# Kernel optimization log

Hardware: AMD Instinct MI355X
Metric: run time of the kernel (lower is better)

## Reference

```python
import jax, jax.numpy as jnp
import numpy as np

B, N, LATENT, HIDDEN = 65536, 32, 32, 64

def setup_inputs() -> dict:
    key = jax.random.key(0)
    ks = jax.random.split(key, 16)
    def xavier(k, shape):
        fan_in, fan_out = shape[1], shape[0]
        lim = float(np.sqrt(6.0 / (fan_in + fan_out)))
        return jax.random.uniform(k, shape, jnp.float32, -lim, lim)
    inp = {
        'x_sensors': jax.random.normal(ks[0], (B, N), jnp.float32),
        'state_x': jax.random.uniform(ks[1], (B, 1), jnp.float32),
        # GAT: W Linear(1, LATENT, bias=False), a Linear(2*LATENT, 1, bias=False), xavier init
        'W_gat': xavier(ks[2], (LATENT, 1)),
        'a_gat': xavier(ks[3], (1, 2 * LATENT)),
        # pooling: Linear(LATENT, LATENT//2) -> Tanh -> Linear(LATENT//2, 1) -> Softmax(dim=1)
        'p1_w': xavier(ks[4], (LATENT // 2, LATENT)),
        'p1_b': jnp.zeros((LATENT // 2,), jnp.float32),
        'p2_w': xavier(ks[5], (1, LATENT // 2)),
        'p2_b': jnp.zeros((1,), jnp.float32),
        # MNN: MonotonicLinear raw weights uniform(-0.5, 0.5), zero bias
        'm1_w': jax.random.uniform(ks[6], (HIDDEN, 1), jnp.float32, -0.5, 0.5),
        'm1_b': jnp.zeros((HIDDEN,), jnp.float32),
        'm2_w': jax.random.uniform(ks[7], (HIDDEN, HIDDEN), jnp.float32, -0.5, 0.5),
        'm2_b': jnp.zeros((HIDDEN,), jnp.float32),
        'm3_w': jax.random.uniform(ks[8], (LATENT, HIDDEN), jnp.float32, -0.5, 0.5),
        'm3_b': jnp.zeros((LATENT,), jnp.float32),
    }
    return inp

def reference(x_sensors, state_x, W_gat, a_gat, p1_w, p1_b, p2_w, p2_b,
              m1_w, m1_b, m2_w, m2_b, m3_w, m3_b):
    # --- GAT encoder ---
    # h = x_sensors[..., None] (B,N,1); Wh = h @ W_gat.T -> (B,N,D)
    Wh = jnp.einsum('bn,d->bnd', x_sensors, W_gat[:, 0])
    # e_ij = leakyrelu(a^T [Wh_i || Wh_j]) decomposed: a = [a1; a2]
    a1, a2 = a_gat[0, :LATENT], a_gat[0, LATENT:]
    s_i = jnp.einsum('bnd,d->bn', Wh, a1)  # contribution of Wh_i
    s_j = jnp.einsum('bnd,d->bn', Wh, a2)  # contribution of Wh_j
    e = jax.nn.leaky_relu(s_i[:, :, None] + s_j[:, None, :], 0.2)  # (B,N,N)
    alpha = jax.nn.softmax(e, axis=2)  # dropout is identity in eval
    h_prime = jnp.einsum('bij,bjd->bid', alpha, Wh)  # (B,N,D)
    # pooling: softmax over sensor dim (dim=1)
    t = jnp.tanh(h_prime @ p1_w.T + p1_b)
    beta = jax.nn.softmax(t @ p2_w.T + p2_b, axis=1)  # (B,N,1)
    z_enc = jnp.sum(h_prime * beta, axis=1)  # (B,D)
    # --- MNN decoder (exp-positive weights) ---
    h1 = jnp.tanh(state_x @ jnp.exp(m1_w).T + m1_b)
    h2 = jnp.tanh(h1 @ jnp.exp(m2_w).T + m2_b)
    z_dec = h2 @ jnp.exp(m3_w).T + m3_b  # (B,D)
    return (z_enc, z_dec)
```

## Files before the change

### kernel.cpp

```cpp
#include <hip/hip_runtime.h>
#include <hip/hip_bf16.h>

#define LOG2E     1.4426950408889634f
#define TWO_LOG2E 2.8853900817779268f

typedef __attribute__((ext_vector_type(8))) _Float16 f16x8;
typedef __attribute__((ext_vector_type(4))) float    f32x4;
typedef __attribute__((ext_vector_type(2))) float    f32x2;

__device__ __forceinline__ float rcp_(float x){ return __builtin_amdgcn_rcpf(x); }
__device__ __forceinline__ float ex2_(float x){ return __builtin_amdgcn_exp2f(x); }

template<int K>
__device__ __forceinline__ float quadbc(float v){
  constexpr int ctrl = K * 0x55;
  return __int_as_float(__builtin_amdgcn_mov_dpp(__float_as_int(v), ctrl, 0xf, 0xf, true));
}

union FragH { f16x8 v; uint32_t w[4]; uint4 u4; };

__device__ __forceinline__ uint32_t pkh(float a, float b){
  union { _Float16 h; uint16_t u; } ca, cb;
  ca.h = (_Float16)a; cb.h = (_Float16)b;
  return (uint32_t)ca.u | ((uint32_t)cb.u << 16);
}
__device__ __forceinline__ void exph8(const float* __restrict__ src, FragH& out){
  float4 a = *(const float4*)src;
  float4 b = *(const float4*)(src + 4);
  out.w[0] = pkh(__expf(a.x), __expf(a.y));
  out.w[1] = pkh(__expf(a.z), __expf(a.w));
  out.w[2] = pkh(__expf(b.x), __expf(b.y));
  out.w[3] = pkh(__expf(b.z), __expf(b.w));
}

#define WS_FG1   0
#define WS_FG2   2048
#define WS_TBL   3072
#define WS_E1S   3584
#define WS_M1B   3648
#define WS_SCAL  3712

#define TBL_N     512
#define TBL_SCALE 25.6f
#define TBL_LO    -10.0f
#define TBL_CMAX  9.9f

__global__ __launch_bounds__(256) void IDSSM_pre(
    const float* __restrict__ Wg,  const float* __restrict__ ag,
    const float* __restrict__ p1w, const float* __restrict__ p1b,
    const float* __restrict__ p2w, const float* __restrict__ p2b,
    const float* __restrict__ m1w, const float* __restrict__ m1b,
    const float* __restrict__ m2w, const float* __restrict__ m3w,
    float* __restrict__ ws)
{
  const int blk = blockIdx.x;
  const int tid = threadIdx.x;
  const int l  = tid & 63;
  const int bl = l & 15, gt = l >> 4;
  if (blk < 2){
    const int s  = (blk*256 + tid) >> 6;
    const int mt = s >> 1, kt = s & 1;
    FragH h;
    exph8(m2w + (bl + 16*mt)*64 + 8*gt + 32*kt, h);
    *(uint4*)(ws + WS_FG1 + (size_t)(s*64 + l)*4) = h.u4;
  } else if (blk == 2){
    const int s2  = tid >> 6;
    const int mt2 = s2 >> 1, kt2 = s2 & 1;
    FragH h;
    exph8(m3w + (bl + 16*mt2)*64 + 8*gt + 32*kt2, h);
    *(uint4*)(ws + WS_FG2 + (size_t)(s2*64 + l)*4) = h.u4;
  } else if (blk == 3){
    __shared__ float qs[16], pb_[16], pw[16], u0s[1];
    if (tid < 16){
      float acc = 0.f;
      #pragma unroll
      for (int d = 0; d < 32; ++d) acc += p1w[tid*32 + d] * Wg[d];
      qs[tid]  = acc * TWO_LOG2E;
      pb_[tid] = p1b[tid] * TWO_LOG2E;
      pw[tid]  = -2.f * p2w[tid];
    }
    if (tid == 16){
      float sp = 0.f;
      #pragma unroll
      for (int k = 0; k < 16; ++k) sp += p2w[k];
      u0s[0] = sp + p2b[0];
    }
    __syncthreads();
    #pragma unroll
    for (int rep = 0; rep < 2; ++rep){
      const int n = tid + rep*256;
      const float c = TBL_LO + (float)n * (1.0f/TBL_SCALE);
      float u = u0s[0];
      #pragma unroll
      for (int k = 0; k < 16; ++k){
        float E = ex2_(fmaf(c, qs[k], pb_[k]));
        u = fmaf(pw[k], rcp_(E + 1.f), u);
      }
      ws[WS_TBL + n] = u * LOG2E;
    }
  } else {
    if (tid < 64){
      ws[WS_E1S + tid] = __expf(m1w[tid]) * TWO_LOG2E;
      ws[WS_M1B + tid] = m1b[tid] * TWO_LOG2E;
    } else if (tid == 64){
      float A1 = 0.f, A2 = 0.f;
      #pragma unroll
      for (int d = 0; d < 32; ++d){ A1 += Wg[d]*ag[d]; A2 += Wg[d]*ag[32+d]; }
      ws[WS_SCAL + 0] = A1 * LOG2E;
      ws[WS_SCAL + 1] = A2 * LOG2E;
    }
  }
}

#define EATT_J(SX, SF, SQ, JQ, JR) { \
    const float Fj_ = quadbc<JQ>(SF[JR]); \
    const float Fq_ = quadbc<JQ>(SQ[JR]); \
    const float xj_ = quadbc<JQ>(SX[JR]); \
    const f32x2 Fj2_ = {Fj_,Fj_}, Fq2_ = {Fq_,Fq_}, xj2_ = {xj_,xj_}; \
    f32x2 pe_; \
    pe_ = __builtin_elementwise_max(Ei2[0]*Fj2_, Eq2[0]*Fq2_); s2[0] = s2[0] + pe_; sx2[0] = sx2[0] + pe_*xj2_; \
    pe_ = __builtin_elementwise_max(Ei2[1]*Fj2_, Eq2[1]*Fq2_); s2[1] = s2[1] + pe_; sx2[1] = sx2[1] + pe_*xj2_; \
  }
#define EATT_Q(SX, SF, SQ, JQ) \
    EATT_J(SX,SF,SQ,JQ,0) EATT_J(SX,SF,SQ,JQ,1) EATT_J(SX,SF,SQ,JQ,2) EATT_J(SX,SF,SQ,JQ,3)
#define EATT_ALL(SX, SF, SQ) \
    EATT_Q(SX,SF,SQ,0) EATT_Q(SX,SF,SQ,1) EATT_Q(SX,SF,SQ,2) EATT_Q(SX,SF,SQ,3)

__global__ __launch_bounds__(256, 6) void IDSSM_main(
    const float* __restrict__ xs,  const float* __restrict__ stx,
    const float* __restrict__ Wg,  const float* __restrict__ m2b,
    const float* __restrict__ m3b, const float* __restrict__ ws,
    float* __restrict__ out, int B)
{
  __shared__ float tbl[TBL_N];
  const int tid = threadIdx.x;
  const int lb  = tid >> 3;
  const int r   = tid & 7;
  const int b0  = blockIdx.x * 32;
  const int b   = b0 + lb;
  const bool valid = (b < B);
  const int rsrc = valid ? b : (B - 1);

  const float2 tco = *(const float2*)(ws + WS_TBL + tid*2);
  tbl[tid*2]     = tco.x;
  tbl[tid*2 + 1] = tco.y;

  const float A1p = ws[WS_SCAL + 0];
  const float A2p = ws[WS_SCAL + 1];

  const float4 xv = *(const float4*)(xs + (size_t)rsrc*32 + r*4);
  float xi[4] = { xv.x, xv.y, xv.z, xv.w };

  float Fjr[4], Fqr[4];
  #pragma unroll
  for (int t = 0; t < 4; ++t){
    const float tv = A2p * xi[t];
    Fjr[t] = ex2_(tv);
    Fqr[t] = ex2_(0.2f * tv);
  }
  float xo[4], Fo[4], Fqo[4];
  #pragma unroll
  for (int t = 0; t < 4; ++t){
    xo[t]  = __shfl_xor(xi[t], 4);
    Fo[t]  = __shfl_xor(Fjr[t], 4);
    Fqo[t] = __shfl_xor(Fqr[t], 4);
  }

  f32x2 Ei2[2], Eq2[2], s2[2], sx2[2];
  #pragma unroll
  for (int p = 0; p < 2; ++p){
    const float sa = A1p * xi[2*p], sb = A1p * xi[2*p + 1];
    Ei2[p] = (f32x2){ ex2_(sa), ex2_(sb) };
    Eq2[p] = (f32x2){ ex2_(0.2f*sa), ex2_(0.2f*sb) };
    s2[p]  = (f32x2)(0.f);
    sx2[p] = (f32x2)(0.f);
  }
  EATT_ALL(xi, Fjr, Fqr)
  EATT_ALL(xo, Fo,  Fqo)

  __syncthreads();

  float Zs = 0.f, Zd = 0.f;
  #pragma unroll
  for (int p = 0; p < 2; ++p){
    #pragma unroll
    for (int h = 0; h < 2; ++h){
      const float sv  = h ? s2[p].y  : s2[p].x;
      const float sxv = h ? sx2[p].y : sx2[p].x;
      const float c  = sxv * rcp_(sv);
      const float cc = fminf(fmaxf(c, TBL_LO), TBL_CMAX);
      const float f  = (cc - TBL_LO) * TBL_SCALE;
      const int   n  = (int)f;
      const float fr = f - (float)n;
      const float t0 = tbl[n];
      const float t1 = tbl[n + 1];
      const float eb = ex2_(fmaf(fr, t1 - t0, t0));
      Zs = fmaf(eb, c, Zs);
      Zd += eb;
    }
  }
  Zs += __shfl_xor(Zs, 1);  Zd += __shfl_xor(Zd, 1);
  Zs += __shfl_xor(Zs, 2);  Zd += __shfl_xor(Zd, 2);
  Zs += __shfl_xor(Zs, 4);  Zd += __shfl_xor(Zd, 4);
  const float Z = Zs * rcp_(Zd);

  if (valid){
    const float4 w = ((const float4*)Wg)[r];
    *(float4*)(out + (size_t)b*32 + r*4) =
        make_float4(Z*w.x, Z*w.y, Z*w.z, Z*w.w);
  }

  const int wv = tid >> 6;
  if (wv >= 2) return;

  const int lane = tid & 63;
  const int gt   = lane >> 4;
  const int bl   = lane & 15;
  const int bd   = b0 + wv*16 + bl;
  const float sx0 = stx[(bd < B) ? bd : (B-1)];

  uint4 fg1r[8];
  #pragma unroll
  for (int s = 0; s < 8; ++s)
    fg1r[s] = *(const uint4*)(ws + WS_FG1 + (size_t)(s*64 + lane)*4);

  FragH h1f[2];
  #pragma unroll
  for (int kt = 0; kt < 2; ++kt){
    const int g0 = 8*gt + 32*kt;
    const float4* e1p = (const float4*)(ws + WS_E1S + g0);
    const float4* m1p = (const float4*)(ws + WS_M1B + g0);
    float4 ea = e1p[0], eb4 = e1p[1];
    float4 ma = m1p[0], mb4 = m1p[1];
    float ev[8] = { ea.x,ea.y,ea.z,ea.w, eb4.x,eb4.y,eb4.z,eb4.w };
    float mv[8] = { ma.x,ma.y,ma.z,ma.w, mb4.x,mb4.y,mb4.z,mb4.w };
    float hv[8];
    #pragma unroll
    for (int j = 0; j < 8; ++j){
      float E = ex2_(fmaf(sx0, ev[j], mv[j]));
      hv[j] = fmaf(-2.f, rcp_(E + 1.f), 1.f);
    }
    #pragma unroll
    for (int jw = 0; jw < 4; ++jw)
      h1f[kt].w[jw] = pkh(hv[2*jw], hv[2*jw+1]);
  }

  f32x4 acc[4];
  #pragma unroll
  for (int mt = 0; mt < 4; ++mt){
    float4 bi = *(const float4*)(m2b + 16*mt + 4*gt);
    acc[mt][0]=bi.x; acc[mt][1]=bi.y; acc[mt][2]=bi.z; acc[mt][3]=bi.w;
  }
  #pragma unroll
  for (int mt = 0; mt < 4; ++mt){
    #pragma unroll
    for (int kt = 0; kt < 2; ++kt){
      FragH A; A.u4 = fg1r[mt*2 + kt];
      acc[mt] = __builtin_amdgcn_mfma_f32_16x16x32_f16(A.v, h1f[kt].v, acc[mt], 0, 0, 0);
    }
  }

  uint4 fg2r[4];
  #pragma unroll
  for (int s = 0; s < 4; ++s)
    fg2r[s] = *(const uint4*)(ws + WS_FG2 + (size_t)(s*64 + lane)*4);

  uint32_t Wp[4][2];
  #pragma unroll
  for (int mt = 0; mt < 4; ++mt){
    float t0 = fmaf(-2.f, rcp_(ex2_(acc[mt][0]*TWO_LOG2E) + 1.f), 1.f);
    float t1 = fmaf(-2.f, rcp_(ex2_(acc[mt][1]*TWO_LOG2E) + 1.f), 1.f);
    float t2 = fmaf(-2.f, rcp_(ex2_(acc[mt][2]*TWO_LOG2E) + 1.f), 1.f);
    float t3 = fmaf(-2.f, rcp_(ex2_(acc[mt][3]*TWO_LOG2E) + 1.f), 1.f);
    Wp[mt][0] = pkh(t0, t1);
    Wp[mt][1] = pkh(t2, t3);
  }

  FragH B2[2];
  const int hiSel = gt >> 1;
  #pragma unroll
  for (int kt2 = 0; kt2 < 2; ++kt2){
    #pragma unroll
    for (int jw = 0; jw < 4; ++jw){
      const int sl = bl + 16*(((jw>>1) + 2*gt) & 3);
      const int w  = jw & 1;
      uint32_t c0 = (uint32_t)__shfl((int)Wp[2*kt2+0][w], sl);
      uint32_t c1 = (uint32_t)__shfl((int)Wp[2*kt2+1][w], sl);
      B2[kt2].w[jw] = hiSel ? c1 : c0;
    }
  }

  f32x4 acc2[2];
  #pragma unroll
  for (int mt2 = 0; mt2 < 2; ++mt2){
    float4 bi = *(const float4*)(m3b + 16*mt2 + 4*gt);
    acc2[mt2][0]=bi.x; acc2[mt2][1]=bi.y; acc2[mt2][2]=bi.z; acc2[mt2][3]=bi.w;
  }
  #pragma unroll
  for (int mt2 = 0; mt2 < 2; ++mt2){
    #pragma unroll
    for (int kt2 = 0; kt2 < 2; ++kt2){
      FragH A; A.u4 = fg2r[mt2*2 + kt2];
      acc2[mt2] = __builtin_amdgcn_mfma_f32_16x16x32_f16(A.v, B2[kt2].v, acc2[mt2], 0, 0, 0);
    }
  }

  if (bd < B){
    float* o = out + (size_t)B*32 + (size_t)bd*32;
    *(float4*)(o + 4*gt)      = make_float4(acc2[0][0], acc2[0][1], acc2[0][2], acc2[0][3]);
    *(float4*)(o + 16 + 4*gt) = make_float4(acc2[1][0], acc2[1][1], acc2[1][2], acc2[1][3]);
  }
}

extern "C" void kernel_launch(void* const* d_in, const int* in_sizes, int n_in,
                              void* d_out, int out_size, void* d_ws, size_t ws_size,
                              hipStream_t stream)
{
  const float* xs  = (const float*)d_in[0];
  const float* stx = (const float*)d_in[1];
  const float* Wg  = (const float*)d_in[2];
  const float* ag  = (const float*)d_in[3];
  const float* p1w = (const float*)d_in[4];
  const float* p1b = (const float*)d_in[5];
  const float* p2w = (const float*)d_in[6];
  const float* p2b = (const float*)d_in[7];
  const float* m1w = (const float*)d_in[8];
  const float* m1b = (const float*)d_in[9];
  const float* m2w = (const float*)d_in[10];
  const float* m2b = (const float*)d_in[11];
  const float* m3w = (const float*)d_in[12];
  const float* m3b = (const float*)d_in[13];
  float* out = (float*)d_out;
  float* ws  = (float*)d_ws;
  const int B = in_sizes[0] / 32;

  hipLaunchKernelGGL(IDSSM_pre, dim3(5), dim3(256), 0, stream,
                     Wg, ag, p1w, p1b, p2w, p2b, m1w, m1b, m2w, m3w, ws);
  const int nblk = (B + 31) / 32;
  hipLaunchKernelGGL(IDSSM_main, dim3(nblk), dim3(256), 0, stream,
                     xs, stx, Wg, m2b, m3b, ws, out, B);
}
```

Measured before the change: 26.95 us.

## Drop shared-memory table and reduce register pressure for higher occupancy

Removes the LDS copy of the interpolation table and the __syncthreads, so lookups read the workspace table straight from global memory through the cache. The shuffled neighbour values now overwrite the local arrays instead of living in separate ones, and the MFMA weight fragments are loaded just before use instead of being prefetched into register arrays. Launch bounds go from 6 to 8 blocks per SM to exploit the lower register use. The trade-off is gather loads from global/L1 in place of LDS reads, and less latency hiding for the fragment loads.

```diff
diff --git a/kernel.cpp b/kernel.cpp
--- a/kernel.cpp
+++ b/kernel.cpp
@@ -112,27 +112,24 @@
   }
 }
 
-#define EATT_J(SX, SF, SQ, JQ, JR) { \
-    const float Fj_ = quadbc<JQ>(SF[JR]); \
-    const float Fq_ = quadbc<JQ>(SQ[JR]); \
-    const float xj_ = quadbc<JQ>(SX[JR]); \
+#define EATT_J(JQ, JR) { \
+    const float Fj_ = quadbc<JQ>(Fjr[JR]); \
+    const float Fq_ = quadbc<JQ>(Fqr[JR]); \
+    const float xj_ = quadbc<JQ>(xi[JR]); \
     const f32x2 Fj2_ = {Fj_,Fj_}, Fq2_ = {Fq_,Fq_}, xj2_ = {xj_,xj_}; \
     f32x2 pe_; \
     pe_ = __builtin_elementwise_max(Ei2[0]*Fj2_, Eq2[0]*Fq2_); s2[0] = s2[0] + pe_; sx2[0] = sx2[0] + pe_*xj2_; \
     pe_ = __builtin_elementwise_max(Ei2[1]*Fj2_, Eq2[1]*Fq2_); s2[1] = s2[1] + pe_; sx2[1] = sx2[1] + pe_*xj2_; \
   }
-#define EATT_Q(SX, SF, SQ, JQ) \
-    EATT_J(SX,SF,SQ,JQ,0) EATT_J(SX,SF,SQ,JQ,1) EATT_J(SX,SF,SQ,JQ,2) EATT_J(SX,SF,SQ,JQ,3)
-#define EATT_ALL(SX, SF, SQ) \
-    EATT_Q(SX,SF,SQ,0) EATT_Q(SX,SF,SQ,1) EATT_Q(SX,SF,SQ,2) EATT_Q(SX,SF,SQ,3)
-
-__global__ __launch_bounds__(256, 6) void IDSSM_main(
+#define EATT_Q(JQ) EATT_J(JQ,0) EATT_J(JQ,1) EATT_J(JQ,2) EATT_J(JQ,3)
+#define EATT_ALL   EATT_Q(0) EATT_Q(1) EATT_Q(2) EATT_Q(3)
+
+__global__ __launch_bounds__(256, 8) void IDSSM_main(
     const float* __restrict__ xs,  const float* __restrict__ stx,
     const float* __restrict__ Wg,  const float* __restrict__ m2b,
     const float* __restrict__ m3b, const float* __restrict__ ws,
     float* __restrict__ out, int B)
 {
-  __shared__ float tbl[TBL_N];
   const int tid = threadIdx.x;
   const int lb  = tid >> 3;
   const int r   = tid & 7;
@@ -141,10 +138,6 @@
   const bool valid = (b < B);
   const int rsrc = valid ? b : (B - 1);
 
-  const float2 tco = *(const float2*)(ws + WS_TBL + tid*2);
-  tbl[tid*2]     = tco.x;
-  tbl[tid*2 + 1] = tco.y;
-
   const float A1p = ws[WS_SCAL + 0];
   const float A2p = ws[WS_SCAL + 1];
 
@@ -157,13 +150,6 @@
     const float tv = A2p * xi[t];
     Fjr[t] = ex2_(tv);
     Fqr[t] = ex2_(0.2f * tv);
-  }
-  float xo[4], Fo[4], Fqo[4];
-  #pragma unroll
-  for (int t = 0; t < 4; ++t){
-    xo[t]  = __shfl_xor(xi[t], 4);
-    Fo[t]  = __shfl_xor(Fjr[t], 4);
-    Fqo[t] = __shfl_xor(Fqr[t], 4);
   }
 
   f32x2 Ei2[2], Eq2[2], s2[2], sx2[2];
@@ -175,11 +161,16 @@
     s2[p]  = (f32x2)(0.f);
     sx2[p] = (f32x2)(0.f);
   }
-  EATT_ALL(xi, Fjr, Fqr)
-  EATT_ALL(xo, Fo,  Fqo)
-
-  __syncthreads();
-
+  EATT_ALL
+  #pragma unroll
+  for (int t = 0; t < 4; ++t){
+    xi[t]  = __shfl_xor(xi[t], 4);
+    Fjr[t] = __shfl_xor(Fjr[t], 4);
+    Fqr[t] = __shfl_xor(Fqr[t], 4);
+  }
+  EATT_ALL
+
+  const float* wt = ws + WS_TBL;
   float Zs = 0.f, Zd = 0.f;
   #pragma unroll
   for (int p = 0; p < 2; ++p){
@@ -192,8 +183,8 @@
       const float f  = (cc - TBL_LO) * TBL_SCALE;
       const int   n  = (int)f;
       const float fr = f - (float)n;
-      const float t0 = tbl[n];
-      const float t1 = tbl[n + 1];
+      const float t0 = wt[n];
+      const float t1 = wt[n + 1];
       const float eb = ex2_(fmaf(fr, t1 - t0, t0));
       Zs = fmaf(eb, c, Zs);
       Zd += eb;
@@ -218,11 +209,6 @@
   const int bl   = lane & 15;
   const int bd   = b0 + wv*16 + bl;
   const float sx0 = stx[(bd < B) ? bd : (B-1)];
-
-  uint4 fg1r[8];
-  #pragma unroll
-  for (int s = 0; s < 8; ++s)
-    fg1r[s] = *(const uint4*)(ws + WS_FG1 + (size_t)(s*64 + lane)*4);
 
   FragH h1f[2];
   #pragma unroll
@@ -255,15 +241,11 @@
   for (int mt = 0; mt < 4; ++mt){
     #pragma unroll
     for (int kt = 0; kt < 2; ++kt){
-      FragH A; A.u4 = fg1r[mt*2 + kt];
+      FragH A;
+      A.u4 = *(const uint4*)(ws + WS_FG1 + (size_t)((mt*2 + kt)*64 + lane)*4);
       acc[mt] = __builtin_amdgcn_mfma_f32_16x16x32_f16(A.v, h1f[kt].v, acc[mt], 0, 0, 0);
     }
   }
-
-  uint4 fg2r[4];
-  #pragma unroll
-  for (int s = 0; s < 4; ++s)
-    fg2r[s] = *(const uint4*)(ws + WS_FG2 + (size_t)(s*64 + lane)*4);
 
   uint32_t Wp[4][2];
   #pragma unroll
@@ -300,7 +282,8 @@
   for (int mt2 = 0; mt2 < 2; ++mt2){
     #pragma unroll
     for (int kt2 = 0; kt2 < 2; ++kt2){
-      FragH A; A.u4 = fg2r[mt2*2 + kt2];
+      FragH A;
+      A.u4 = *(const uint4*)(ws + WS_FG2 + (size_t)((mt2*2 + kt2)*64 + lane)*4);
       acc2[mt2] = __builtin_amdgcn_mfma_f32_16x16x32_f16(A.v, B2[kt2].v, acc2[mt2], 0, 0, 0);
     }
   }
```

After: 68.03 us. 2.52x slower.

## Process 64 batch rows per block with 4 threads per row

Applied to the files above, without the earlier changes.

Each block now covers 64 batch rows, with 4 threads per row instead of 8. Each thread handles 8 query sensors and reads the whole 32-wide row from memory directly, instead of exchanging values across lanes with shuffles. All four waves now run the MNN decoder instead of only two, which halves the number of blocks and the table setup work per row. In exchange each thread holds more registers (the full row plus 8 accumulators), and occupancy hints drop from 6 to 4 blocks per CU.

```diff
diff --git a/kernel.cpp b/kernel.cpp
--- a/kernel.cpp
+++ b/kernel.cpp
@@ -112,21 +112,24 @@
   }
 }
 
-#define EATT_J(SX, SF, SQ, JQ, JR) { \
-    const float Fj_ = quadbc<JQ>(SF[JR]); \
-    const float Fq_ = quadbc<JQ>(SQ[JR]); \
-    const float xj_ = quadbc<JQ>(SX[JR]); \
+#define XJ(J) (((((J)&3))==0) ? xr4[(J)>>2].x : ((((J)&3))==1) ? xr4[(J)>>2].y : \
+               ((((J)&3))==2) ? xr4[(J)>>2].z : xr4[(J)>>2].w)
+
+#define ATT_J(JQ, JR) { \
+    const float Fj_ = quadbc<JQ>(Fjr[JR]); \
+    const float Fq_ = quadbc<JQ>(Fqr[JR]); \
+    const float xj_ = XJ(JQ*8+JR); \
     const f32x2 Fj2_ = {Fj_,Fj_}, Fq2_ = {Fq_,Fq_}, xj2_ = {xj_,xj_}; \
     f32x2 pe_; \
     pe_ = __builtin_elementwise_max(Ei2[0]*Fj2_, Eq2[0]*Fq2_); s2[0] = s2[0] + pe_; sx2[0] = sx2[0] + pe_*xj2_; \
     pe_ = __builtin_elementwise_max(Ei2[1]*Fj2_, Eq2[1]*Fq2_); s2[1] = s2[1] + pe_; sx2[1] = sx2[1] + pe_*xj2_; \
-  }
-#define EATT_Q(SX, SF, SQ, JQ) \
-    EATT_J(SX,SF,SQ,JQ,0) EATT_J(SX,SF,SQ,JQ,1) EATT_J(SX,SF,SQ,JQ,2) EATT_J(SX,SF,SQ,JQ,3)
-#define EATT_ALL(SX, SF, SQ) \
-    EATT_Q(SX,SF,SQ,0) EATT_Q(SX,SF,SQ,1) EATT_Q(SX,SF,SQ,2) EATT_Q(SX,SF,SQ,3)
-
-__global__ __launch_bounds__(256, 6) void IDSSM_main(
+    pe_ = __builtin_elementwise_max(Ei2[2]*Fj2_, Eq2[2]*Fq2_); s2[2] = s2[2] + pe_; sx2[2] = sx2[2] + pe_*xj2_; \
+    pe_ = __builtin_elementwise_max(Ei2[3]*Fj2_, Eq2[3]*Fq2_); s2[3] = s2[3] + pe_; sx2[3] = sx2[3] + pe_*xj2_; \
+  }
+#define ATT_Q(JQ) ATT_J(JQ,0) ATT_J(JQ,1) ATT_J(JQ,2) ATT_J(JQ,3) \
+                  ATT_J(JQ,4) ATT_J(JQ,5) ATT_J(JQ,6) ATT_J(JQ,7)
+
+__global__ __launch_bounds__(256, 4) void IDSSM_main(
     const float* __restrict__ xs,  const float* __restrict__ stx,
     const float* __restrict__ Wg,  const float* __restrict__ m2b,
     const float* __restrict__ m3b, const float* __restrict__ ws,
@@ -134,55 +137,50 @@
 {
   __shared__ float tbl[TBL_N];
   const int tid = threadIdx.x;
-  const int lb  = tid >> 3;
-  const int r   = tid & 7;
-  const int b0  = blockIdx.x * 32;
+  const int lb  = tid >> 2;
+  const int q   = tid & 3;
+  const int b0  = blockIdx.x * 64;
   const int b   = b0 + lb;
   const bool valid = (b < B);
   const int rsrc = valid ? b : (B - 1);
 
   const float2 tco = *(const float2*)(ws + WS_TBL + tid*2);
+  const float A1p = ws[WS_SCAL + 0];
+  const float A2p = ws[WS_SCAL + 1];
+
+  const float4* xrow4 = (const float4*)(xs + (size_t)rsrc*32);
+  float4 xr4[8];
+  #pragma unroll
+  for (int t = 0; t < 8; ++t) xr4[t] = xrow4[t];
+  float4 xia = xrow4[q*2], xib = xrow4[q*2 + 1];
+  float xi[8] = { xia.x, xia.y, xia.z, xia.w, xib.x, xib.y, xib.z, xib.w };
+
   tbl[tid*2]     = tco.x;
   tbl[tid*2 + 1] = tco.y;
 
-  const float A1p = ws[WS_SCAL + 0];
-  const float A2p = ws[WS_SCAL + 1];
-
-  const float4 xv = *(const float4*)(xs + (size_t)rsrc*32 + r*4);
-  float xi[4] = { xv.x, xv.y, xv.z, xv.w };
-
-  float Fjr[4], Fqr[4];
-  #pragma unroll
-  for (int t = 0; t < 4; ++t){
+  float Fjr[8], Fqr[8];
+  #pragma unroll
+  for (int t = 0; t < 8; ++t){
     const float tv = A2p * xi[t];
     Fjr[t] = ex2_(tv);
     Fqr[t] = ex2_(0.2f * tv);
   }
-  float xo[4], Fo[4], Fqo[4];
-  #pragma unroll
-  for (int t = 0; t < 4; ++t){
-    xo[t]  = __shfl_xor(xi[t], 4);
-    Fo[t]  = __shfl_xor(Fjr[t], 4);
-    Fqo[t] = __shfl_xor(Fqr[t], 4);
-  }
-
-  f32x2 Ei2[2], Eq2[2], s2[2], sx2[2];
-  #pragma unroll
-  for (int p = 0; p < 2; ++p){
+  f32x2 Ei2[4], Eq2[4], s2[4], sx2[4];
+  #pragma unroll
+  for (int p = 0; p < 4; ++p){
     const float sa = A1p * xi[2*p], sb = A1p * xi[2*p + 1];
     Ei2[p] = (f32x2){ ex2_(sa), ex2_(sb) };
     Eq2[p] = (f32x2){ ex2_(0.2f*sa), ex2_(0.2f*sb) };
     s2[p]  = (f32x2)(0.f);
     sx2[p] = (f32x2)(0.f);
   }
-  EATT_ALL(xi, Fjr, Fqr)
-  EATT_ALL(xo, Fo,  Fqo)
+  ATT_Q(0) ATT_Q(1) ATT_Q(2) ATT_Q(3)
 
   __syncthreads();
 
   float Zs = 0.f, Zd = 0.f;
   #pragma unroll
-  for (int p = 0; p < 2; ++p){
+  for (int p = 0; p < 4; ++p){
     #pragma unroll
     for (int h = 0; h < 2; ++h){
       const float sv  = h ? s2[p].y  : s2[p].x;
@@ -201,19 +199,18 @@
   }
   Zs += __shfl_xor(Zs, 1);  Zd += __shfl_xor(Zd, 1);
   Zs += __shfl_xor(Zs, 2);  Zd += __shfl_xor(Zd, 2);
-  Zs += __shfl_xor(Zs, 4);  Zd += __shfl_xor(Zd, 4);
   const float Z = Zs * rcp_(Zd);
 
   if (valid){
-    const float4 w = ((const float4*)Wg)[r];
-    *(float4*)(out + (size_t)b*32 + r*4) =
-        make_float4(Z*w.x, Z*w.y, Z*w.z, Z*w.w);
-  }
-
-  const int wv = tid >> 6;
-  if (wv >= 2) return;
+    const float4 w0 = ((const float4*)Wg)[q*2 + 0];
+    const float4 w1 = ((const float4*)Wg)[q*2 + 1];
+    float4* o = (float4*)(out + (size_t)b*32 + q*8);
+    o[0] = make_float4(Z*w0.x, Z*w0.y, Z*w0.z, Z*w0.w);
+    o[1] = make_float4(Z*w1.x, Z*w1.y, Z*w1.z, Z*w1.w);
+  }
 
   const int lane = tid & 63;
+  const int wv   = tid >> 6;
   const int gt   = lane >> 4;
   const int bl   = lane & 15;
   const int bd   = b0 + wv*16 + bl;
@@ -336,7 +333,7 @@
 
   hipLaunchKernelGGL(IDSSM_pre, dim3(5), dim3(256), 0, stream,
                      Wg, ag, p1w, p1b, p2w, p2b, m1w, m1b, m2w, m3w, ws);
-  const int nblk = (B + 31) / 32;
+  const int nblk = (B + 63) / 64;
   hipLaunchKernelGGL(IDSSM_main, dim3(nblk), dim3(256), 0, stream,
                      xs, stx, Wg, m2b, m3b, ws, out, B);
 }
```

New measurement: 24.54 us. 8.9% less time.
